# Optimization experiments

Measured on AMD Instinct MI355X. Metric: run time of the kernel, lower is better.

The kernel has to match this reference:

```python
import jax, jax.numpy as jnp
from jax import lax
import numpy as np

B, T, NL = 512, 64, 32          # batch, timepoints per patient, n_labs
LAT, HID = 64, 128              # latent_dim, hidden_dim
SCALE, STEP, QPAD, TMAX = 365.0, 0.05, 2000, 2000


def setup_inputs() -> dict:
    key = jax.random.key(0)
    k = jax.random.split(key, 24)
    def rn(ki, shape, s=0.05):
        return jax.random.normal(ki, shape, jnp.float32) * s
    Din = 2 * NL + 1  # GRU input: labs, mask, dt
    return {
        "obs_vals": rn(k[0], (B, T, NL), 1.0),
        "age": jax.random.uniform(k[1], (B,), jnp.float32),
        "eps": rn(k[2], (B, LAT), 1.0),  # reparameterization noise (randn_like)
        "gru_Wih": rn(k[3], (Din, 3 * HID)), "gru_Whh": rn(k[4], (HID, 3 * HID)),
        "gru_bih": jnp.zeros((3 * HID,)), "gru_bhh": jnp.zeros((3 * HID,)),
        "Wmu": rn(k[5], (HID, LAT)), "bmu": jnp.zeros((LAT,)),
        "Wlv": rn(k[6], (HID, LAT)), "blv": jnp.zeros((LAT,)),
        "W1": rn(k[7], (LAT, HID)), "b1": jnp.zeros((HID,)),
        "W2": rn(k[8], (HID, HID)), "b2": jnp.zeros((HID,)),
        "W3": rn(k[9], (HID, LAT)), "b3": jnp.zeros((LAT,)),
        "Wo1": rn(k[10], (LAT, HID)), "bo1": jnp.zeros((HID,)),
        "Wo2": rn(k[11], (HID, NL)), "bo2": jnp.zeros((NL,)),
        "Ws1": rn(k[12], (LAT + 1, HID)), "bs1": jnp.zeros((HID,)),
        "Ws2": rn(k[13], (HID, 2)), "bs2": jnp.zeros((2,)),
        "obs_mask": jax.random.bernoulli(k[14], 0.7, (B, T, NL)),
        "timepoints": jnp.sort(jax.random.randint(k[15], (B, T), 0, TMAX), axis=1).astype(jnp.int32),
        "seq_lens": jax.random.randint(k[16], (B,), 1, T + 1).astype(jnp.int32),
    }


def reference(obs_vals, age, eps, gru_Wih, gru_Whh, gru_bih, gru_bhh,
              Wmu, bmu, Wlv, blv, W1, b1, W2, b2, W3, b3,
              Wo1, bo1, Wo2, bo2, Ws1, bs1, Ws2, bs2,
              obs_mask, timepoints, seq_lens):
    Bv, Tv, Dv = obs_vals.shape
    Hdim = gru_Whh.shape[0]
    tp = timepoints.astype(jnp.float32)

    # ---- RecognitionRNN (GRU over reversed sequence) ----
    dt = jnp.concatenate([jnp.zeros((Bv, 1)), tp[:, 1:] - tp[:, :-1]], axis=1)[..., None]
    maskf = obs_mask.astype(obs_vals.dtype)
    inp = jnp.concatenate([obs_vals * maskf, maskf, dt], axis=-1)  # [B,T,2*NL+1]
    x_seq = jnp.flip(inp, axis=1).transpose(1, 0, 2)  # [T,B,Din]

    def gru_step(h, x):
        gi = x @ gru_Wih + gru_bih
        gh = h @ gru_Whh + gru_bhh
        ir, iz, i_n = jnp.split(gi, 3, axis=-1)
        hr, hz, hn = jnp.split(gh, 3, axis=-1)
        r = jax.nn.sigmoid(ir + hr)
        zg = jax.nn.sigmoid(iz + hz)
        n = jnp.tanh(i_n + r * hn)
        h = (1.0 - zg) * n + zg * h
        return h, None

    h, _ = lax.scan(gru_step, jnp.zeros((Bv, Hdim), obs_vals.dtype), x_seq)
    mu = h @ Wmu + bmu
    logvar = h @ Wlv + blv
    z0 = mu + eps * jnp.exp(0.5 * logvar)  # reparameterize

    # ---- query times (padded unique; timepoints are >= 0 by construction) ----
    qd = jnp.unique(timepoints.reshape(-1), size=QPAD, fill_value=timepoints.max())
    query_t = qd.astype(jnp.float32) / SCALE  # [Q], nondecreasing

    # ---- torchdiffeq fixed-grid rk4 with step_size ----
    qnp = np.asarray(query_t)
    t0, t1 = float(qnp[0]), float(qnp[-1])
    niters = int(np.ceil((t1 - t0) / STEP + 1))
    grid = np.arange(niters) * STEP + t0
    if grid[-1] > t1:
        grid[-1] = t1
    grid = jnp.asarray(grid, jnp.float32)  # [G]

    def ode_f(z):
        return jnp.tanh(jnp.tanh(z @ W1 + b1) @ W2 + b2) @ W3 + b3

    def rk4_step(y, hstep):
        k1 = ode_f(y)
        k2 = ode_f(y + 0.5 * hstep * k1)
        k3 = ode_f(y + 0.5 * hstep * k2)
        k4 = ode_f(y + hstep * k3)
        y2 = y + (hstep / 6.0) * (k1 + 2.0 * k2 + 2.0 * k3 + k4)
        return y2, y2

    _, ys = lax.scan(rk4_step, z0, grid[1:] - grid[:-1])
    ys = jnp.concatenate([z0[None], ys], axis=0)  # [G,B,L]

    # linear interpolation of grid states at query_t (torchdiffeq behavior)
    gi = jnp.clip(jnp.searchsorted(grid, query_t, side="right") - 1, 0, grid.shape[0] - 2)
    tl, tr = grid[gi], grid[gi + 1]
    w = ((query_t - tl) / jnp.where(tr - tl == 0, 1.0, tr - tl))[:, None, None]
    z_traj = ys[gi] * (1.0 - w) + ys[gi + 1] * w  # [Q,B,L]

    # ---- reconstruction loss (vectorized over B,T) ----
    tq = tp / SCALE  # [B,T]
    idx_q = jnp.argmin(jnp.abs(query_t[None, None, :] - tq[:, :, None]), axis=-1)  # [B,T]
    z_bt = z_traj[idx_q, jnp.arange(Bv)[:, None]]  # [B,T,L]
    x_hat = jax.nn.relu(z_bt @ Wo1 + bo1) @ Wo2 + bo2  # [B,T,NL]
    valid = (jnp.arange(Tv)[None, :] < seq_lens[:, None]).astype(obs_vals.dtype)[..., None]
    m = maskf * valid
    n_obs = m.sum()
    recon = jnp.where(n_obs > 0,
                      (m * (x_hat - obs_vals) ** 2).sum() / jnp.maximum(n_obs, 1.0),
                      0.0)

    kl = -0.5 * jnp.mean(jnp.sum(1.0 + logvar - mu ** 2 - jnp.exp(logvar), axis=-1))

    # ---- z_eval at last observed timepoint per patient ----
    last_tp = jnp.take_along_axis(tp, (seq_lens - 1)[:, None], axis=1)[:, 0] / SCALE  # [B]
    idx_e = jnp.argmin(jnp.abs(query_t[None, :] - last_tp[:, None]), axis=-1)  # [B]
    z_eval = z_traj[idx_e, jnp.arange(Bv)]  # [B,L]
    log_hazard = jax.nn.relu(jnp.concatenate([z_eval, age[:, None]], axis=-1) @ Ws1 + bs1) @ Ws2 + bs2
    return log_hazard, recon, kl, z_eval
```

## Files before the change

### kernel.cpp

```cpp
#include <hip/hip_runtime.h>
#include <hip/hip_bf16.h>
#include <math.h>

#define B 512
#define T 64
#define NL 32
#define LAT 64
#define HID 128
#define DIN 65
#define G3 384
#define FSCALE 365.0f
#define MAXGRID 128

#define WS_MIN   0
#define WS_MAX   1
#define WS_NIT   2
#define WS_KL    3
#define WS_RE    4
#define WS_NO    5
#define WS_GRID  8
#define WS_Z0    (WS_GRID + MAXGRID)
#define WS_YS    (WS_Z0 + B*LAT)
#define WS_W31   (WS_YS + 120*B*LAT)
#define WS_B31   (WS_W31 + HID*HID)

typedef __attribute__((ext_vector_type(8))) __bf16 bf16x8;
typedef __attribute__((ext_vector_type(4))) float f32x4;

#define SWZ(row) ((((row)>>3)&1)<<5)

static __device__ __forceinline__ float tanh_fast(float x){
    float t = __builtin_amdgcn_exp2f(x * 2.8853900817779268f);
    return 1.0f - 2.0f * __builtin_amdgcn_rcpf(t + 1.0f);
}
static __device__ __forceinline__ float sigmoid_fast(float x){
    return __builtin_amdgcn_rcpf(1.0f + __builtin_amdgcn_exp2f(-1.4426950408889634f * x));
}
static __device__ __forceinline__ void bar_lds(){
    asm volatile("" ::: "memory");
    asm volatile("s_waitcnt lgkmcnt(0)" ::: "memory");
    __builtin_amdgcn_s_barrier();
    asm volatile("" ::: "memory");
}

__global__ void k_setup(const int* __restrict__ tp, float* wsf){
    int* wsi = (int*)wsf;
    __shared__ int smin[256], smax[256];
    int tid = threadIdx.x;
    int mn = 2147483647, mx = -2147483647-1;
    for (int i = tid; i < B*T; i += 256){ int v = tp[i]; mn = min(mn,v); mx = max(mx,v); }
    smin[tid]=mn; smax[tid]=mx; __syncthreads();
    for (int s=128; s>0; s>>=1){
        if (tid<s){ smin[tid]=min(smin[tid],smin[tid+s]); smax[tid]=max(smax[tid],smax[tid+s]); }
        __syncthreads();
    }
    float t0f = (float)smin[0] / FSCALE;
    float t1f = (float)smax[0] / FSCALE;
    double t0d = (double)t0f, t1d = (double)t1f;
    int nit = (int)ceil((t1d-t0d)/0.05 + 1.0);
    if (nit < 1) nit = 1;
    if (nit > MAXGRID) nit = MAXGRID;
    if (tid==0){
        wsi[WS_NIT] = nit;
        wsf[WS_KL]=0.f; wsf[WS_RE]=0.f; wsf[WS_NO]=0.f;
    }
    if (tid < nit){
        double g = (double)tid * 0.05 + t0d;
        if (tid == nit-1 && g > t1d) g = t1d;
        wsf[WS_GRID + tid] = (float)g;
    }
}

__global__ __launch_bounds__(256) void k_w31(
    const float* __restrict__ W1, const float* __restrict__ W3,
    const float* __restrict__ b3, float* wsf)
{
    int gid = blockIdx.x*256 + threadIdx.x;
    int k = gid >> 5, n0 = (gid & 31)*4;
    float4 acc = {0.f,0.f,0.f,0.f};
    #pragma unroll 8
    for (int l=0;l<64;++l){
        float w3v = W3[k*LAT + l];
        float4 w1v = *(const float4*)&W1[l*HID + n0];
        acc.x = fmaf(w3v, w1v.x, acc.x);
        acc.y = fmaf(w3v, w1v.y, acc.y);
        acc.z = fmaf(w3v, w1v.z, acc.z);
        acc.w = fmaf(w3v, w1v.w, acc.w);
    }
    *(float4*)&wsf[WS_W31 + k*HID + n0] = acc;
    if (blockIdx.x==0 && threadIdx.x < HID){
        int n = threadIdx.x; float a = 0.f;
        #pragma unroll 8
        for (int l=0;l<64;++l) a = fmaf(b3[l], W1[l*HID+n], a);
        wsf[WS_B31 + n] = a;
    }
}

__global__ __launch_bounds__(512) void k_gru(
    const float* __restrict__ obs, const float* __restrict__ eps,
    const float* __restrict__ Wih, const float* __restrict__ Whh,
    const float* __restrict__ bih, const float* __restrict__ bhh,
    const float* __restrict__ Wmu, const float* __restrict__ bmu,
    const float* __restrict__ Wlv, const float* __restrict__ blv,
    const int* __restrict__ maskI, const int* __restrict__ tp,
    float* wsf)
{
    const int b0 = blockIdx.x * 16;
    const int tid = threadIdx.x;
    const int w = tid >> 6, lane = tid & 63;
    const int g = lane >> 4, c = lane & 15;
    const int xr = tid >> 5, xl = tid & 31;

    __shared__ __align__(16) __bf16 xh[16][232];
    __shared__ int   tps[16][64];
    __shared__ float dts[16];
    __shared__ float lvs[16][64];
    __shared__ float red[8];
    char* xbase = (char*)&xh[0][0];
    #define XH_RD(row, bytecol) (*(const bf16x8*)(xbase + (row)*464 + ((bytecol) ^ SWZ(row))))
    #define XH_WPTR(row, bytecol) ((__bf16*)(xbase + (row)*464 + ((bytecol) ^ SWZ(row))))

    ((int2*)tps)[tid] = ((const int2*)(tp + (size_t)b0*T))[tid];
    {
        unsigned* xz = (unsigned*)xbase;
        #pragma unroll
        for (int i=0;i<1856;i+=512) xz[i+tid] = 0u;
    }

    bf16x8 wr[6], wz[6], wi[2], wh[4];
    #pragma unroll
    for (int q=0;q<6;++q){
        int kt = q<2 ? q : q+1;
        #pragma unroll
        for (int e=0;e<8;++e){
            int k = kt*32 + g*8 + e;
            float vr, vz;
            if (k < 64){ vr = Wih[k*G3 + 16*w+c];      vz = Wih[k*G3 + 128+16*w+c]; }
            else       { vr = Whh[(k-96)*G3 + 16*w+c]; vz = Whh[(k-96)*G3 + 128+16*w+c]; }
            wr[q][e] = (__bf16)vr; wz[q][e] = (__bf16)vz;
        }
    }
    #pragma unroll
    for (int q=0;q<2;++q)
        #pragma unroll
        for (int e=0;e<8;++e)
            wi[q][e] = (__bf16)Wih[(q*32+g*8+e)*G3 + 256+16*w+c];
    #pragma unroll
    for (int q=0;q<4;++q)
        #pragma unroll
        for (int e=0;e<8;++e)
            wh[q][e] = (__bf16)Whh[(q*32+g*8+e)*G3 + 256+16*w+c];
    const float wdr = Wih[64*G3 + 16*w+c];
    const float wdz = Wih[64*G3 + 128+16*w+c];
    const float wdn = Wih[64*G3 + 256+16*w+c];
    const float rb  = bih[16*w+c]     + bhh[16*w+c];
    const float zb  = bih[128+16*w+c] + bhh[128+16*w+c];
    const float inb = bih[256+16*w+c];
    const float hnb = bhh[256+16*w+c];

    __syncthreads();

    {
        float mv = (float)maskI[((size_t)(b0+xr)*T + 63)*NL + xl];
        float ov = obs[((size_t)(b0+xr)*T + 63)*NL + xl];
        *XH_WPTR(xr, 2*xl)      = (__bf16)(ov*mv);
        *XH_WPTR(xr, 64 + 2*xl) = (__bf16)mv;
        if (xl==0) dts[xr] = (float)(tps[xr][63]-tps[xr][62]);
    }
    float ovP = 0.f, mvP = 0.f;
    {
        mvP = (float)maskI[((size_t)(b0+xr)*T + 62)*NL + xl];
        ovP = obs[((size_t)(b0+xr)*T + 62)*NL + xl];
    }

    float hold[4] = {0.f,0.f,0.f,0.f};

    for (int s=0;s<T;++s){
        bar_lds();
        bf16x8 A0 = XH_RD(c, 0   + 16*g);
        bf16x8 A1 = XH_RD(c, 64  + 16*g);
        bf16x8 A2 = XH_RD(c, 192 + 16*g);
        bf16x8 A3 = XH_RD(c, 256 + 16*g);
        bf16x8 A4 = XH_RD(c, 320 + 16*g);
        bf16x8 A5 = XH_RD(c, 384 + 16*g);
        const float dt0=dts[4*g], dt1=dts[4*g+1], dt2=dts[4*g+2], dt3=dts[4*g+3];
        float ovN=0.f, mvN=0.f; const int t2 = 61-s;
        if (t2 >= 0){
            mvN = (float)maskI[((size_t)(b0+xr)*T + t2)*NL + xl];
            ovN = obs[((size_t)(b0+xr)*T + t2)*NL + xl];
        }
        f32x4 racc={0,0,0,0}, zacc={0,0,0,0}, inacc={0,0,0,0}, hnacc={0,0,0,0};
        racc  = __builtin_amdgcn_mfma_f32_16x16x32_bf16(A0, wr[0], racc, 0,0,0);
        zacc  = __builtin_amdgcn_mfma_f32_16x16x32_bf16(A0, wz[0], zacc, 0,0,0);
        inacc = __builtin_amdgcn_mfma_f32_16x16x32_bf16(A0, wi[0], inacc,0,0,0);
        hnacc = __builtin_amdgcn_mfma_f32_16x16x32_bf16(A2, wh[0], hnacc,0,0,0);
        racc  = __builtin_amdgcn_mfma_f32_16x16x32_bf16(A1, wr[1], racc, 0,0,0);
        zacc  = __builtin_amdgcn_mfma_f32_16x16x32_bf16(A1, wz[1], zacc, 0,0,0);
        inacc = __builtin_amdgcn_mfma_f32_16x16x32_bf16(A1, wi[1], inacc,0,0,0);
        hnacc = __builtin_amdgcn_mfma_f32_16x16x32_bf16(A3, wh[1], hnacc,0,0,0);
        racc  = __builtin_amdgcn_mfma_f32_16x16x32_bf16(A2, wr[2], racc, 0,0,0);
        zacc  = __builtin_amdgcn_mfma_f32_16x16x32_bf16(A2, wz[2], zacc, 0,0,0);
        hnacc = __builtin_amdgcn_mfma_f32_16x16x32_bf16(A4, wh[2], hnacc,0,0,0);
        racc  = __builtin_amdgcn_mfma_f32_16x16x32_bf16(A3, wr[3], racc, 0,0,0);
        zacc  = __builtin_amdgcn_mfma_f32_16x16x32_bf16(A3, wz[3], zacc, 0,0,0);
        hnacc = __builtin_amdgcn_mfma_f32_16x16x32_bf16(A5, wh[3], hnacc,0,0,0);
        racc  = __builtin_amdgcn_mfma_f32_16x16x32_bf16(A4, wr[4], racc, 0,0,0);
        zacc  = __builtin_amdgcn_mfma_f32_16x16x32_bf16(A4, wz[4], zacc, 0,0,0);
        racc  = __builtin_amdgcn_mfma_f32_16x16x32_bf16(A5, wr[5], racc, 0,0,0);
        zacc  = __builtin_amdgcn_mfma_f32_16x16x32_bf16(A5, wz[5], zacc, 0,0,0);
        float hnew[4]; const float dtv[4] = {dt0,dt1,dt2,dt3};
        #pragma unroll
        for (int j=0;j<4;++j){
            float dv = dtv[j];
            float r  = sigmoid_fast(racc[j] + rb + dv*wdr);
            float zg = sigmoid_fast(zacc[j] + zb + dv*wdz);
            float n  = tanh_fast(inacc[j] + inb + dv*wdn + r*(hnacc[j] + hnb));
            float hv = (1.f - zg)*n + zg*hold[j];
            hold[j] = hv; hnew[j] = hv;
        }
        bar_lds();
        #pragma unroll
        for (int j=0;j<4;++j)
            *XH_WPTR(4*g+j, 192 + 2*(16*w+c)) = (__bf16)hnew[j];
        if (s < T-1){
            const int tn = 62 - s;
            *XH_WPTR(xr, 2*xl)      = (__bf16)(ovP*mvP);
            *XH_WPTR(xr, 64 + 2*xl) = (__bf16)mvP;
            if (xl==0) dts[xr] = (tn>0) ? (float)(tps[xr][tn]-tps[xr][tn-1]) : 0.f;
        }
        ovP = ovN; mvP = mvN;
    }
    __syncthreads();

    const int col4 = 16*(w&3)+c;
    bf16x8 Ah0 = XH_RD(c, 192 + 0   + 16*g);
    bf16x8 Ah1 = XH_RD(c, 192 + 64  + 16*g);
    bf16x8 Ah2 = XH_RD(c, 192 + 128 + 16*g);
    bf16x8 Ah3 = XH_RD(c, 192 + 192 + 16*g);
    const float* Wm = (w<4)? Wmu : Wlv;
    f32x4 acc={0,0,0,0};
    {
        bf16x8 bf0,bf1,bf2,bf3;
        #pragma unroll
        for (int e=0;e<8;++e){
            bf0[e] = (__bf16)Wm[(0*32+g*8+e)*LAT + col4];
            bf1[e] = (__bf16)Wm[(1*32+g*8+e)*LAT + col4];
            bf2[e] = (__bf16)Wm[(2*32+g*8+e)*LAT + col4];
            bf3[e] = (__bf16)Wm[(3*32+g*8+e)*LAT + col4];
        }
        acc = __builtin_amdgcn_mfma_f32_16x16x32_bf16(Ah0, bf0, acc, 0,0,0);
        acc = __builtin_amdgcn_mfma_f32_16x16x32_bf16(Ah1, bf1, acc, 0,0,0);
        acc = __builtin_amdgcn_mfma_f32_16x16x32_bf16(Ah2, bf2, acc, 0,0,0);
        acc = __builtin_amdgcn_mfma_f32_16x16x32_bf16(Ah3, bf3, acc, 0,0,0);
    }
    const float mbias = (w<4)? bmu[col4] : blv[col4];
    if (w>=4){
        #pragma unroll
        for (int j=0;j<4;++j) lvs[4*g+j][col4] = acc[j] + mbias;
    }
    __syncthreads();
    if (w<4){
        float kl = 0.f;
        #pragma unroll
        for (int j=0;j<4;++j){
            float mu = acc[j] + mbias;
            float lv = lvs[4*g+j][col4];
            int row = b0 + 4*g + j;
            float z0 = mu + eps[(size_t)row*LAT + col4]*expf(0.5f*lv);
            wsf[WS_Z0 + (size_t)row*LAT + col4] = z0;
            wsf[WS_YS + (size_t)row*LAT + col4] = z0;
            kl += 1.f + lv - mu*mu - expf(lv);
        }
        #pragma unroll
        for (int off=32; off>0; off>>=1) kl += __shfl_xor(kl, off);
        if (lane==0) red[w] = kl;
    }
    __syncthreads();
    if (tid==0) atomicAdd(&wsf[WS_KL], red[0]+red[1]+red[2]+red[3]);
    #undef XH_RD
    #undef XH_WPTR
}

__global__ __launch_bounds__(512) void k_ode(
    const float* __restrict__ W1, const float* __restrict__ b1,
    const float* __restrict__ W2, const float* __restrict__ b2,
    const float* __restrict__ W3, const float* __restrict__ b3,
    float* wsf)
{
    const int b0 = blockIdx.x * 16;
    const int tid = threadIdx.x;
    const int w = tid >> 6, lane = tid & 63;
    const int g = lane >> 4, c = lane & 15;
    const int hc = 16*w + c;
    const int lc = 16*(w&3) + c;
    const int* wsi = (const int*)wsf;
    const int nit = wsi[WS_NIT];

    __shared__ __align__(16) __bf16 Gl[16][136];
    __shared__ __align__(16) __bf16 Hl[16][136];
    __shared__ float gls[MAXGRID];
    char* gbase = (char*)&Gl[0][0];
    char* hbase = (char*)&Hl[0][0];
    #define LDS_RD(base, row, bytecol) (*(const bf16x8*)((base) + (row)*272 + ((bytecol) ^ SWZ(row))))
    #define LDS_WPTR(base, row, bytecol) ((__bf16*)((base) + (row)*272 + ((bytecol) ^ SWZ(row))))

    bf16x8 w2f[4], w31f[4], w3f[4];
    #pragma unroll
    for (int q=0;q<4;++q)
        #pragma unroll
        for (int e=0;e<8;++e){
            w2f[q][e]  = (__bf16)W2[(q*32+g*8+e)*HID + hc];
            w31f[q][e] = (__bf16)wsf[WS_W31 + (q*32+g*8+e)*HID + hc];
            w3f[q][e]  = (__bf16)W3[(q*32+g*8+e)*LAT + lc];
        }
    const float b1v  = b1[hc];
    const float b2v  = b2[hc];
    const float b31v = wsf[WS_B31 + hc];
    const float b3v  = b3[lc];

    for (int kk=tid; kk<MAXGRID; kk+=512) gls[kk]=wsf[WS_GRID+kk];

    {
        int r = tid >> 5, l0 = (tid & 31)*2;
        float2 zv = *(const float2*)&wsf[WS_Z0 + (size_t)(b0+r)*LAT + l0];
        __bf16* p = LDS_WPTR(gbase, r, 2*l0);
        p[0] = (__bf16)zv.x;
        p[1] = (__bf16)zv.y;
    }
    float y[4];
    #pragma unroll
    for (int j=0;j<4;++j)
        y[j] = wsf[WS_Z0 + (size_t)(b0+4*g+j)*LAT + lc];
    __syncthreads();

    f32x4 U;
    {
        bf16x8 az0 = LDS_RD(gbase, c, 16*g);
        bf16x8 az1 = LDS_RD(gbase, c, 64 + 16*g);
        bf16x8 wf0, wf1;
        #pragma unroll
        for (int e=0;e<8;++e){
            wf0[e] = (__bf16)W1[(g*8+e)*HID + hc];
            wf1[e] = (__bf16)W1[(32+g*8+e)*HID + hc];
        }
        f32x4 a = {0.f,0.f,0.f,0.f};
        a = __builtin_amdgcn_mfma_f32_16x16x32_bf16(az0, wf0, a, 0,0,0);
        a = __builtin_amdgcn_mfma_f32_16x16x32_bf16(az1, wf1, a, 0,0,0);
        U = a;
    }
    __syncthreads();

    #pragma unroll
    for (int j=0;j<4;++j)
        *LDS_WPTR(gbase, 4*g+j, 2*hc) = (__bf16)tanh_fast(U[j] + b1v);
    __syncthreads();

    f32x4 Uacc={0,0,0,0}, faccv={0,0,0,0};

    for (int i=0; i<nit-1; ++i){
        const float h = gls[i+1]-gls[i];
        #pragma unroll
        for (int sub=0; sub<4; ++sub){
            {
                bf16x8 a0 = LDS_RD(gbase, c, 0   + 16*g);
                bf16x8 a1 = LDS_RD(gbase, c, 64  + 16*g);
                bf16x8 a2 = LDS_RD(gbase, c, 128 + 16*g);
                bf16x8 a3 = LDS_RD(gbase, c, 192 + 16*g);
                __builtin_amdgcn_s_setprio(1);
                f32x4 ca={0,0,0,0}, cb={0,0,0,0};
                ca = __builtin_amdgcn_mfma_f32_16x16x32_bf16(a0, w2f[0], ca, 0,0,0);
                cb = __builtin_amdgcn_mfma_f32_16x16x32_bf16(a2, w2f[2], cb, 0,0,0);
                ca = __builtin_amdgcn_mfma_f32_16x16x32_bf16(a1, w2f[1], ca, 0,0,0);
                cb = __builtin_amdgcn_mfma_f32_16x16x32_bf16(a3, w2f[3], cb, 0,0,0);
                __builtin_amdgcn_s_setprio(0);
                #pragma unroll
                for (int j=0;j<4;++j)
                    *LDS_WPTR(hbase, 4*g+j, 2*hc) = (__bf16)tanh_fast(ca[j]+cb[j]+b2v);
            }
            bar_lds();
            {
                bf16x8 h0 = LDS_RD(hbase, c, 0   + 16*g);
                bf16x8 h1 = LDS_RD(hbase, c, 64  + 16*g);
                bf16x8 h2 = LDS_RD(hbase, c, 128 + 16*g);
                bf16x8 h3 = LDS_RD(hbase, c, 192 + 16*g);
                __builtin_amdgcn_s_setprio(1);
                f32x4 va={0,0,0,0}, vb={0,0,0,0};
                va = __builtin_amdgcn_mfma_f32_16x16x32_bf16(h0, w31f[0], va, 0,0,0);
                vb = __builtin_amdgcn_mfma_f32_16x16x32_bf16(h2, w31f[2], vb, 0,0,0);
                va = __builtin_amdgcn_mfma_f32_16x16x32_bf16(h1, w31f[1], va, 0,0,0);
                vb = __builtin_amdgcn_mfma_f32_16x16x32_bf16(h3, w31f[3], vb, 0,0,0);
                f32x4 fv = {0,0,0,0};
                if (w < 4){
                    f32x4 fa={0,0,0,0}, fb={0,0,0,0};
                    fa = __builtin_amdgcn_mfma_f32_16x16x32_bf16(h0, w3f[0], fa, 0,0,0);
                    fb = __builtin_amdgcn_mfma_f32_16x16x32_bf16(h2, w3f[2], fb, 0,0,0);
                    fa = __builtin_amdgcn_mfma_f32_16x16x32_bf16(h1, w3f[1], fa, 0,0,0);
                    fb = __builtin_amdgcn_mfma_f32_16x16x32_bf16(h3, w3f[3], fb, 0,0,0);
                    #pragma unroll
                    for (int j=0;j<4;++j) fv[j] = fa[j] + fb[j] + b3v;
                }
                __builtin_amdgcn_s_setprio(0);
                f32x4 V;
                #pragma unroll
                for (int j=0;j<4;++j) V[j] = va[j] + vb[j] + b31v;

                if (sub==0){ Uacc = V; faccv = fv; }
                else if (sub==3){ Uacc += V; faccv += fv; }
                else { Uacc += 2.f*V; faccv += 2.f*fv; }

                if (sub < 3){
                    const float al = (sub==2) ? h : 0.5f*h;
                    #pragma unroll
                    for (int j=0;j<4;++j)
                        *LDS_WPTR(gbase, 4*g+j, 2*hc) = (__bf16)tanh_fast(fmaf(al, V[j], U[j]) + b1v);
                } else {
                    const float h6 = h*(1.0f/6.0f);
                    if (w < 4){
                        #pragma unroll
                        for (int j=0;j<4;++j){
                            y[j] = fmaf(h6, faccv[j], y[j]);
                            wsf[WS_YS + ((size_t)(i+1)*B + (b0+4*g+j))*LAT + lc] = y[j];
                        }
                    }
                    #pragma unroll
                    for (int j=0;j<4;++j){
                        U[j] = fmaf(h6, Uacc[j], U[j]);
                        *LDS_WPTR(gbase, 4*g+j, 2*hc) = (__bf16)tanh_fast(U[j] + b1v);
                    }
                }
            }
            bar_lds();
        }
    }
    #undef LDS_RD
    #undef LDS_WPTR
}

__global__ __launch_bounds__(512) void k_recon(
    const float* __restrict__ obs, const int* __restrict__ maskI,
    const int* __restrict__ tp, const int* __restrict__ seq,
    const float* __restrict__ Wo1, const float* __restrict__ bo1,
    const float* __restrict__ Wo2, const float* __restrict__ bo2,
    const float* __restrict__ age,
    const float* __restrict__ Ws1, const float* __restrict__ bs1,
    const float* __restrict__ Ws2, const float* __restrict__ bs2,
    float* wsf, float* out)
{
    const int b = blockIdx.x, tid = threadIdx.x;
    const int w = tid >> 6, lane = tid & 63;
    const int g = lane >> 4, c = lane & 15;
    __shared__ __align__(16) __bf16 zbt[64][72];
    __shared__ __align__(16) __bf16 hb[64][136];
    __shared__ float gls[MAXGRID];
    __shared__ float red[16];
    __shared__ float ze[64];
    __shared__ float pred[4];
    const int* wsi=(const int*)wsf;
    const int nit = wsi[WS_NIT];
    for (int i=tid;i<MAXGRID;i+=512) gls[i]=wsf[WS_GRID+i];

    bf16x8 wo1f[2], wo2f[4];
    #pragma unroll
    for (int q=0;q<2;++q)
        #pragma unroll
        for (int e=0;e<8;++e)
            wo1f[q][e] = (__bf16)Wo1[(q*32+g*8+e)*HID + 16*w+c];
    {
        int n = w & 1;
        #pragma unroll
        for (int q=0;q<4;++q)
            #pragma unroll
            for (int e=0;e<8;++e)
                wo2f[q][e] = (__bf16)Wo2[(q*32+g*8+e)*NL + 16*n+c];
    }
    const float bo1v = bo1[16*w+c];
    const float bo2v = bo2[16*(w&1)+c];
    const int sl = seq[b];
    __syncthreads();

    {
        int t = tid >> 3, seg = tid & 7;
        float tq = (float)tp[b*T+t] / FSCALE;
        int lo=0, hi=nit;
        while (lo<hi){ int mid=(lo+hi)>>1; if (gls[mid]<=tq) lo=mid+1; else hi=mid; }
        int k = lo-1; if (k<0) k=0; if (nit>=2 && k>nit-2) k=nit-2; if (nit<2) k=0;
        float wq=0.f;
        if (nit>=2){ float tl=gls[k], tr=gls[k+1]; float den=(tr-tl==0.f)?1.f:(tr-tl); wq=(tq-tl)/den; }
        size_t o0 = (size_t)WS_YS + ((size_t)k*B + b)*LAT + seg*8;
        float4 za0 = *(const float4*)&wsf[o0];
        float4 za1 = *(const float4*)&wsf[o0+4];
        float4 zb0, zb1;
        if (nit>=2){
            zb0 = *(const float4*)&wsf[o0 + (size_t)B*LAT];
            zb1 = *(const float4*)&wsf[o0 + (size_t)B*LAT + 4];
        } else { zb0 = za0; zb1 = za1; }
        __bf16* dst = &zbt[t][seg*8];
        dst[0] = (__bf16)(za0.x*(1.f-wq)+zb0.x*wq);
        dst[1] = (__bf16)(za0.y*(1.f-wq)+zb0.y*wq);
        dst[2] = (__bf16)(za0.z*(1.f-wq)+zb0.z*wq);
        dst[3] = (__bf16)(za0.w*(1.f-wq)+zb0.w*wq);
        dst[4] = (__bf16)(za1.x*(1.f-wq)+zb1.x*wq);
        dst[5] = (__bf16)(za1.y*(1.f-wq)+zb1.y*wq);
        dst[6] = (__bf16)(za1.z*(1.f-wq)+zb1.z*wq);
        dst[7] = (__bf16)(za1.w*(1.f-wq)+zb1.w*wq);
    }
    __syncthreads();

    #pragma unroll
    for (int m=0;m<4;++m){
        f32x4 acc = {0.f,0.f,0.f,0.f};
        bf16x8 a0 = *(const bf16x8*)&zbt[16*m+c][g*8];
        bf16x8 a1 = *(const bf16x8*)&zbt[16*m+c][32+g*8];
        acc = __builtin_amdgcn_mfma_f32_16x16x32_bf16(a0, wo1f[0], acc, 0,0,0);
        acc = __builtin_amdgcn_mfma_f32_16x16x32_bf16(a1, wo1f[1], acc, 0,0,0);
        #pragma unroll
        for (int j=0;j<4;++j)
            hb[16*m+4*g+j][16*w+c] = (__bf16)fmaxf(acc[j] + bo1v, 0.f);
    }
    __syncthreads();

    float esum = 0.f, ncnt = 0.f;
    {
        int m = w >> 1, n = w & 1;
        f32x4 ca = {0.f,0.f,0.f,0.f}, cb = {0.f,0.f,0.f,0.f};
        bf16x8 a0 = *(const bf16x8*)&hb[16*m+c][g*8];
        bf16x8 a1 = *(const bf16x8*)&hb[16*m+c][32+g*8];
        bf16x8 a2 = *(const bf16x8*)&hb[16*m+c][64+g*8];
        bf16x8 a3 = *(const bf16x8*)&hb[16*m+c][96+g*8];
        ca = __builtin_amdgcn_mfma_f32_16x16x32_bf16(a0, wo2f[0], ca, 0,0,0);
        cb = __builtin_amdgcn_mfma_f32_16x16x32_bf16(a2, wo2f[2], cb, 0,0,0);
        ca = __builtin_amdgcn_mfma_f32_16x16x32_bf16(a1, wo2f[1], ca, 0,0,0);
        cb = __builtin_amdgcn_mfma_f32_16x16x32_bf16(a3, wo2f[3], cb, 0,0,0);
        #pragma unroll
        for (int j=0;j<4;++j){
            int t = 16*m + 4*g + j;
            int col = 16*n + c;
            float xh2 = (ca[j]+cb[j]) + bo2v;
            float mv = (float)maskI[(b*T+t)*NL+col] * ((t<sl)?1.f:0.f);
            float d = xh2 - obs[(b*T+t)*NL+col];
            esum = fmaf(mv*d, d, esum);
            ncnt += mv;
        }
    }
    #pragma unroll
    for (int off=32; off>0; off>>=1){
        esum += __shfl_xor(esum, off);
        ncnt += __shfl_xor(ncnt, off);
    }
    if (lane==0){ red[w] = esum; red[8+w] = ncnt; }
    __syncthreads();
    if (tid==0){
        float s=0.f, nn=0.f;
        #pragma unroll
        for (int i=0;i<8;++i){ s += red[i]; nn += red[8+i]; }
        atomicAdd(&wsf[WS_RE], s);
        atomicAdd(&wsf[WS_NO], nn);
    }

    {
        float tq = (float)tp[b*T + sl-1] / FSCALE;
        int lo=0,hi=nit;
        while(lo<hi){int mid=(lo+hi)>>1; if (gls[mid]<=tq) lo=mid+1; else hi=mid;}
        int k=lo-1; if(k<0)k=0; if(nit>=2 && k>nit-2)k=nit-2; if (nit<2) k=0;
        float wq=0.f;
        if (nit>=2){ float tl=gls[k],tr=gls[k+1]; float den=(tr-tl==0.f)?1.f:(tr-tl); wq=(tq-tl)/den; }
        if (tid<LAT){
            size_t o0 = (size_t)WS_YS + ((size_t)k*B+b)*LAT+tid;
            float zl = wsf[o0]*(1.f-wq) + ((nit>=2)? wsf[o0+(size_t)B*LAT]*wq : 0.f);
            ze[tid]=zl;
            out[1026 + b*LAT + tid] = zl;
        }
        __syncthreads();
        if (tid < 128){
            float hj = bs1[tid];
            #pragma unroll 8
            for (int l=0;l<LAT;++l) hj = fmaf(ze[l], Ws1[l*HID+tid], hj);
            hj = fmaf(age[b], Ws1[LAT*HID+tid], hj);
            hj = fmaxf(hj,0.f);
            float p0 = hj*Ws2[tid*2+0], p1 = hj*Ws2[tid*2+1];
            #pragma unroll
            for (int off=32;off>0;off>>=1){ p0 += __shfl_down(p0,off); p1 += __shfl_down(p1,off); }
            int wv = tid>>6;
            if ((tid&63)==0){ pred[wv*2]=p0; pred[wv*2+1]=p1; }
        }
        __syncthreads();
        if (tid==0){
            out[b*2+0] = bs2[0] + pred[0]+pred[2];
            out[b*2+1] = bs2[1] + pred[1]+pred[3];
        }
    }
}

__global__ void k_fin(float* wsf, float* out){
    float n = wsf[WS_NO];
    out[1024] = (n>0.f) ? (wsf[WS_RE]/fmaxf(n,1.f)) : 0.f;
    out[1025] = -0.5f * (wsf[WS_KL] / (float)B);
}

extern "C" void kernel_launch(void* const* d_in, const int* in_sizes, int n_in,
                              void* d_out, int out_size, void* d_ws, size_t ws_size,
                              hipStream_t stream) {
    const float* obs   = (const float*)d_in[0];
    const float* age   = (const float*)d_in[1];
    const float* eps   = (const float*)d_in[2];
    const float* Wih   = (const float*)d_in[3];
    const float* Whh   = (const float*)d_in[4];
    const float* bih   = (const float*)d_in[5];
    const float* bhh   = (const float*)d_in[6];
    const float* Wmu   = (const float*)d_in[7];
    const float* bmu   = (const float*)d_in[8];
    const float* Wlv   = (const float*)d_in[9];
    const float* blv   = (const float*)d_in[10];
    const float* W1    = (const float*)d_in[11];
    const float* b1    = (const float*)d_in[12];
    const float* W2    = (const float*)d_in[13];
    const float* b2    = (const float*)d_in[14];
    const float* W3    = (const float*)d_in[15];
    const float* b3    = (const float*)d_in[16];
    const float* Wo1   = (const float*)d_in[17];
    const float* bo1   = (const float*)d_in[18];
    const float* Wo2   = (const float*)d_in[19];
    const float* bo2   = (const float*)d_in[20];
    const float* Ws1   = (const float*)d_in[21];
    const float* bs1   = (const float*)d_in[22];
    const float* Ws2   = (const float*)d_in[23];
    const float* bs2   = (const float*)d_in[24];
    const int*   maskI = (const int*)d_in[25];
    const int*   tp    = (const int*)d_in[26];
    const int*   seq   = (const int*)d_in[27];
    float* wsf = (float*)d_ws;
    float* out = (float*)d_out;

    k_setup<<<1, 256, 0, stream>>>(tp, wsf);
    k_w31<<<16, 256, 0, stream>>>(W1, W3, b3, wsf);
    k_gru<<<B/16, 512, 0, stream>>>(obs, eps, Wih, Whh, bih, bhh, Wmu, bmu, Wlv, blv,
                                    maskI, tp, wsf);
    k_ode<<<B/16, 512, 0, stream>>>(W1, b1, W2, b2, W3, b3, wsf);
    k_recon<<<B, 512, 0, stream>>>(obs, maskI, tp, seq, Wo1, bo1, Wo2, bo2,
                                   age, Ws1, bs1, Ws2, bs2, wsf, out);
    k_fin<<<1, 1, 0, stream>>>(wsf, out);
}
```

Baseline: 527.8 us.

## Prepack bf16 weight fragments in a prep kernel and fold finalize into recon

Merges the setup and W3·W1 product kernels into one prep kernel that also converts the GRU, ODE and recon weights into bf16 MFMA fragment layouts in the workspace. The main kernels then load their fragments with one contiguous 16-byte read per thread instead of many strided scalar global loads and conversions per block. The separate finalize kernel is removed: the last recon block, found through an atomic counter, writes the loss scalars. This cuts two kernel launches and the redundant per-block weight gathering. It adds a workspace dependency, and the combined W31 is now rounded to bf16 in a different order.

```diff
diff --git a/kernel.cpp b/kernel.cpp
--- a/kernel.cpp
+++ b/kernel.cpp
@@ -12,17 +12,19 @@
 #define FSCALE 365.0f
 #define MAXGRID 128
 
-#define WS_MIN   0
-#define WS_MAX   1
 #define WS_NIT   2
 #define WS_KL    3
 #define WS_RE    4
 #define WS_NO    5
+#define WS_CNT   6
 #define WS_GRID  8
 #define WS_Z0    (WS_GRID + MAXGRID)
 #define WS_YS    (WS_Z0 + B*LAT)
-#define WS_W31   (WS_YS + 120*B*LAT)
-#define WS_B31   (WS_W31 + HID*HID)
+#define FR_BASE  (WS_YS + 112*B*LAT)
+#define GRU_FR   FR_BASE
+#define ODE_FR   (GRU_FR + 18*512*4)
+#define REC_FR   (ODE_FR + 14*512*4)
+#define WS_B31   (WS_YS + 120*B*LAT)
 
 typedef __attribute__((ext_vector_type(8))) __bf16 bf16x8;
 typedef __attribute__((ext_vector_type(4))) float f32x4;
@@ -43,63 +45,146 @@
     asm volatile("" ::: "memory");
 }
 
-__global__ void k_setup(const int* __restrict__ tp, float* wsf){
+__global__ __launch_bounds__(256) void k_prep(
+    const int* __restrict__ tp,
+    const float* __restrict__ Wih, const float* __restrict__ Whh,
+    const float* __restrict__ W1,  const float* __restrict__ W2,
+    const float* __restrict__ W3,  const float* __restrict__ b3,
+    const float* __restrict__ Wo1, const float* __restrict__ Wo2,
+    float* wsf)
+{
     int* wsi = (int*)wsf;
-    __shared__ int smin[256], smax[256];
-    int tid = threadIdx.x;
-    int mn = 2147483647, mx = -2147483647-1;
-    for (int i = tid; i < B*T; i += 256){ int v = tp[i]; mn = min(mn,v); mx = max(mx,v); }
-    smin[tid]=mn; smax[tid]=mx; __syncthreads();
-    for (int s=128; s>0; s>>=1){
-        if (tid<s){ smin[tid]=min(smin[tid],smin[tid+s]); smax[tid]=max(smax[tid],smax[tid+s]); }
-        __syncthreads();
-    }
-    float t0f = (float)smin[0] / FSCALE;
-    float t1f = (float)smax[0] / FSCALE;
-    double t0d = (double)t0f, t1d = (double)t1f;
-    int nit = (int)ceil((t1d-t0d)/0.05 + 1.0);
-    if (nit < 1) nit = 1;
-    if (nit > MAXGRID) nit = MAXGRID;
-    if (tid==0){
-        wsi[WS_NIT] = nit;
-        wsf[WS_KL]=0.f; wsf[WS_RE]=0.f; wsf[WS_NO]=0.f;
-    }
-    if (tid < nit){
-        double g = (double)tid * 0.05 + t0d;
-        if (tid == nit-1 && g > t1d) g = t1d;
-        wsf[WS_GRID + tid] = (float)g;
-    }
-}
-
-__global__ __launch_bounds__(256) void k_w31(
-    const float* __restrict__ W1, const float* __restrict__ W3,
-    const float* __restrict__ b3, float* wsf)
-{
-    int gid = blockIdx.x*256 + threadIdx.x;
-    int k = gid >> 5, n0 = (gid & 31)*4;
-    float4 acc = {0.f,0.f,0.f,0.f};
-    #pragma unroll 8
-    for (int l=0;l<64;++l){
-        float w3v = W3[k*LAT + l];
-        float4 w1v = *(const float4*)&W1[l*HID + n0];
-        acc.x = fmaf(w3v, w1v.x, acc.x);
-        acc.y = fmaf(w3v, w1v.y, acc.y);
-        acc.z = fmaf(w3v, w1v.z, acc.z);
-        acc.w = fmaf(w3v, w1v.w, acc.w);
-    }
-    *(float4*)&wsf[WS_W31 + k*HID + n0] = acc;
-    if (blockIdx.x==0 && threadIdx.x < HID){
-        int n = threadIdx.x; float a = 0.f;
+    const int tid = threadIdx.x;
+    if (blockIdx.x == 8){
+        __shared__ int smin[256], smax[256];
+        int mn = 2147483647, mx = -2147483647-1;
+        for (int i = tid; i < B*T; i += 256){ int v = tp[i]; mn = min(mn,v); mx = max(mx,v); }
+        smin[tid]=mn; smax[tid]=mx; __syncthreads();
+        for (int s=128; s>0; s>>=1){
+            if (tid<s){ smin[tid]=min(smin[tid],smin[tid+s]); smax[tid]=max(smax[tid],smax[tid+s]); }
+            __syncthreads();
+        }
+        float t0f = (float)smin[0] / FSCALE;
+        float t1f = (float)smax[0] / FSCALE;
+        double t0d = (double)t0f, t1d = (double)t1f;
+        int nit = (int)ceil((t1d-t0d)/0.05 + 1.0);
+        if (nit < 1) nit = 1;
+        if (nit > MAXGRID) nit = MAXGRID;
+        if (tid==0){
+            wsi[WS_NIT] = nit; wsi[WS_CNT] = 0;
+            wsf[WS_KL]=0.f; wsf[WS_RE]=0.f; wsf[WS_NO]=0.f;
+        }
+        if (tid < nit){
+            double g = (double)tid * 0.05 + t0d;
+            if (tid == nit-1 && g > t1d) g = t1d;
+            wsf[WS_GRID + tid] = (float)g;
+        }
+        return;
+    }
+    const int w = blockIdx.x;
+    const int qp = tid >> 6;
+    const int lane = tid & 63;
+    const int g = lane >> 4, c = lane & 15;
+    const int hc = 16*w + c;
+    const int lc = 16*(w&3) + c;
+    const int role = w*64 + lane;
+    __shared__ float W1l[64][HID];
+    __shared__ float W3l[HID][64];
+    for (int i = tid; i < 64*HID/4; i += 256)
+        ((float4*)&W1l[0][0])[i] = ((const float4*)W1)[i];
+    for (int i = tid; i < HID*64/4; i += 256)
+        ((float4*)&W3l[0][0])[i] = ((const float4*)W3)[i];
+    __syncthreads();
+
+    {
+        int qlist[2]; int nq = 0;
+        qlist[nq++] = qp;
+        if (qp < 2) qlist[nq++] = 4+qp;
+        for (int ii=0; ii<nq; ++ii){
+            int q = qlist[ii];
+            int kt = q<2 ? q : q+1;
+            bf16x8 vr8, vz8;
+            #pragma unroll
+            for (int e=0;e<8;++e){
+                int k = kt*32 + g*8 + e;
+                float vr, vz;
+                if (k < 64){ vr = Wih[k*G3 + hc];      vz = Wih[k*G3 + 128+hc]; }
+                else       { vr = Whh[(k-96)*G3 + hc]; vz = Whh[(k-96)*G3 + 128+hc]; }
+                vr8[e] = (__bf16)vr; vz8[e] = (__bf16)vz;
+            }
+            *(bf16x8*)&wsf[GRU_FR + ((q)*512 + role)*4]   = vr8;
+            *(bf16x8*)&wsf[GRU_FR + ((6+q)*512 + role)*4] = vz8;
+        }
+    }
+    if (qp < 2){
+        bf16x8 v;
+        #pragma unroll
+        for (int e=0;e<8;++e) v[e] = (__bf16)Wih[(qp*32+g*8+e)*G3 + 256+hc];
+        *(bf16x8*)&wsf[GRU_FR + ((12+qp)*512 + role)*4] = v;
+    }
+    {
+        bf16x8 v;
+        #pragma unroll
+        for (int e=0;e<8;++e) v[e] = (__bf16)Whh[(qp*32+g*8+e)*G3 + 256+hc];
+        *(bf16x8*)&wsf[GRU_FR + ((14+qp)*512 + role)*4] = v;
+    }
+    {
+        bf16x8 v;
+        #pragma unroll
+        for (int e=0;e<8;++e) v[e] = (__bf16)W2[(qp*32+g*8+e)*HID + hc];
+        *(bf16x8*)&wsf[ODE_FR + ((qp)*512 + role)*4] = v;
+    }
+    {
+        bf16x8 v;
+        #pragma unroll
+        for (int e=0;e<8;++e){
+            int k = qp*32 + g*8 + e;
+            float a0=0.f, a1=0.f;
+            #pragma unroll 4
+            for (int l=0;l<64;l+=2){
+                a0 = fmaf(W3l[k][l],   W1l[l][hc],   a0);
+                a1 = fmaf(W3l[k][l+1], W1l[l+1][hc], a1);
+            }
+            v[e] = (__bf16)(a0+a1);
+        }
+        *(bf16x8*)&wsf[ODE_FR + ((4+qp)*512 + role)*4] = v;
+    }
+    {
+        bf16x8 v;
+        #pragma unroll
+        for (int e=0;e<8;++e) v[e] = (__bf16)W3l[qp*32+g*8+e][lc];
+        *(bf16x8*)&wsf[ODE_FR + ((8+qp)*512 + role)*4] = v;
+    }
+    if (qp < 2){
+        bf16x8 v;
+        #pragma unroll
+        for (int e=0;e<8;++e) v[e] = (__bf16)W1l[qp*32+g*8+e][hc];
+        *(bf16x8*)&wsf[ODE_FR + ((12+qp)*512 + role)*4] = v;
+    }
+    if (qp < 2){
+        bf16x8 v;
+        #pragma unroll
+        for (int e=0;e<8;++e) v[e] = (__bf16)Wo1[(qp*32+g*8+e)*HID + hc];
+        *(bf16x8*)&wsf[REC_FR + ((qp)*512 + role)*4] = v;
+    }
+    {
+        bf16x8 v;
+        #pragma unroll
+        for (int e=0;e<8;++e) v[e] = (__bf16)Wo2[(qp*32+g*8+e)*NL + 16*(w&1)+c];
+        *(bf16x8*)&wsf[REC_FR + ((2+qp)*512 + role)*4] = v;
+    }
+    if (qp == 3 && g == 0){
+        float a = 0.f;
         #pragma unroll 8
-        for (int l=0;l<64;++l) a = fmaf(b3[l], W1[l*HID+n], a);
-        wsf[WS_B31 + n] = a;
+        for (int l=0;l<64;++l) a = fmaf(b3[l], W1l[l][hc], a);
+        wsf[WS_B31 + hc] = a;
     }
 }
 
 __global__ __launch_bounds__(512) void k_gru(
     const float* __restrict__ obs, const float* __restrict__ eps,
-    const float* __restrict__ Wih, const float* __restrict__ Whh,
     const float* __restrict__ bih, const float* __restrict__ bhh,
+    const float* __restrict__ Wih,
     const float* __restrict__ Wmu, const float* __restrict__ bmu,
     const float* __restrict__ Wlv, const float* __restrict__ blv,
     const int* __restrict__ maskI, const int* __restrict__ tp,
@@ -128,28 +213,17 @@
     }
 
     bf16x8 wr[6], wz[6], wi[2], wh[4];
-    #pragma unroll
-    for (int q=0;q<6;++q){
-        int kt = q<2 ? q : q+1;
-        #pragma unroll
-        for (int e=0;e<8;++e){
-            int k = kt*32 + g*8 + e;
-            float vr, vz;
-            if (k < 64){ vr = Wih[k*G3 + 16*w+c];      vz = Wih[k*G3 + 128+16*w+c]; }
-            else       { vr = Whh[(k-96)*G3 + 16*w+c]; vz = Whh[(k-96)*G3 + 128+16*w+c]; }
-            wr[q][e] = (__bf16)vr; wz[q][e] = (__bf16)vz;
-        }
-    }
-    #pragma unroll
-    for (int q=0;q<2;++q)
-        #pragma unroll
-        for (int e=0;e<8;++e)
-            wi[q][e] = (__bf16)Wih[(q*32+g*8+e)*G3 + 256+16*w+c];
-    #pragma unroll
-    for (int q=0;q<4;++q)
-        #pragma unroll
-        for (int e=0;e<8;++e)
-            wh[q][e] = (__bf16)Whh[(q*32+g*8+e)*G3 + 256+16*w+c];
+    {
+        const bf16x8* gfr = (const bf16x8*)&wsf[GRU_FR];
+        #pragma unroll
+        for (int q=0;q<6;++q) wr[q] = gfr[q*512 + tid];
+        #pragma unroll
+        for (int q=0;q<6;++q) wz[q] = gfr[(6+q)*512 + tid];
+        #pragma unroll
+        for (int q=0;q<2;++q) wi[q] = gfr[(12+q)*512 + tid];
+        #pragma unroll
+        for (int q=0;q<4;++q) wh[q] = gfr[(14+q)*512 + tid];
+    }
     const float wdr = Wih[64*G3 + 16*w+c];
     const float wdz = Wih[64*G3 + 128+16*w+c];
     const float wdn = Wih[64*G3 + 256+16*w+c];
@@ -282,10 +356,8 @@
 }
 
 __global__ __launch_bounds__(512) void k_ode(
-    const float* __restrict__ W1, const float* __restrict__ b1,
-    const float* __restrict__ W2, const float* __restrict__ b2,
-    const float* __restrict__ W3, const float* __restrict__ b3,
-    float* wsf)
+    const float* __restrict__ b1, const float* __restrict__ b2,
+    const float* __restrict__ b3, float* wsf)
 {
     const int b0 = blockIdx.x * 16;
     const int tid = threadIdx.x;
@@ -304,15 +376,18 @@
     #define LDS_RD(base, row, bytecol) (*(const bf16x8*)((base) + (row)*272 + ((bytecol) ^ SWZ(row))))
     #define LDS_WPTR(base, row, bytecol) ((__bf16*)((base) + (row)*272 + ((bytecol) ^ SWZ(row))))
 
-    bf16x8 w2f[4], w31f[4], w3f[4];
-    #pragma unroll
-    for (int q=0;q<4;++q)
-        #pragma unroll
-        for (int e=0;e<8;++e){
-            w2f[q][e]  = (__bf16)W2[(q*32+g*8+e)*HID + hc];
-            w31f[q][e] = (__bf16)wsf[WS_W31 + (q*32+g*8+e)*HID + hc];
-            w3f[q][e]  = (__bf16)W3[(q*32+g*8+e)*LAT + lc];
-        }
+    bf16x8 w2f[4], w31f[4], w3f[4], w1f0, w1f1;
+    {
+        const bf16x8* ofr = (const bf16x8*)&wsf[ODE_FR];
+        #pragma unroll
+        for (int q=0;q<4;++q) w2f[q]  = ofr[q*512 + tid];
+        #pragma unroll
+        for (int q=0;q<4;++q) w31f[q] = ofr[(4+q)*512 + tid];
+        #pragma unroll
+        for (int q=0;q<4;++q) w3f[q]  = ofr[(8+q)*512 + tid];
+        w1f0 = ofr[12*512 + tid];
+        w1f1 = ofr[13*512 + tid];
+    }
     const float b1v  = b1[hc];
     const float b2v  = b2[hc];
     const float b31v = wsf[WS_B31 + hc];
@@ -337,15 +412,9 @@
     {
         bf16x8 az0 = LDS_RD(gbase, c, 16*g);
         bf16x8 az1 = LDS_RD(gbase, c, 64 + 16*g);
-        bf16x8 wf0, wf1;
-        #pragma unroll
-        for (int e=0;e<8;++e){
-            wf0[e] = (__bf16)W1[(g*8+e)*HID + hc];
-            wf1[e] = (__bf16)W1[(32+g*8+e)*HID + hc];
-        }
         f32x4 a = {0.f,0.f,0.f,0.f};
-        a = __builtin_amdgcn_mfma_f32_16x16x32_bf16(az0, wf0, a, 0,0,0);
-        a = __builtin_amdgcn_mfma_f32_16x16x32_bf16(az1, wf1, a, 0,0,0);
+        a = __builtin_amdgcn_mfma_f32_16x16x32_bf16(az0, w1f0, a, 0,0,0);
+        a = __builtin_amdgcn_mfma_f32_16x16x32_bf16(az1, w1f1, a, 0,0,0);
         U = a;
     }
     __syncthreads();
@@ -439,8 +508,7 @@
 __global__ __launch_bounds__(512) void k_recon(
     const float* __restrict__ obs, const int* __restrict__ maskI,
     const int* __restrict__ tp, const int* __restrict__ seq,
-    const float* __restrict__ Wo1, const float* __restrict__ bo1,
-    const float* __restrict__ Wo2, const float* __restrict__ bo2,
+    const float* __restrict__ bo1, const float* __restrict__ bo2,
     const float* __restrict__ age,
     const float* __restrict__ Ws1, const float* __restrict__ bs1,
     const float* __restrict__ Ws2, const float* __restrict__ bs2,
@@ -460,18 +528,12 @@
     for (int i=tid;i<MAXGRID;i+=512) gls[i]=wsf[WS_GRID+i];
 
     bf16x8 wo1f[2], wo2f[4];
-    #pragma unroll
-    for (int q=0;q<2;++q)
-        #pragma unroll
-        for (int e=0;e<8;++e)
-            wo1f[q][e] = (__bf16)Wo1[(q*32+g*8+e)*HID + 16*w+c];
-    {
-        int n = w & 1;
-        #pragma unroll
-        for (int q=0;q<4;++q)
-            #pragma unroll
-            for (int e=0;e<8;++e)
-                wo2f[q][e] = (__bf16)Wo2[(q*32+g*8+e)*NL + 16*n+c];
+    {
+        const bf16x8* rfr = (const bf16x8*)&wsf[REC_FR];
+        wo1f[0] = rfr[0*512 + tid];
+        wo1f[1] = rfr[1*512 + tid];
+        #pragma unroll
+        for (int q=0;q<4;++q) wo2f[q] = rfr[(2+q)*512 + tid];
     }
     const float bo1v = bo1[16*w+c];
     const float bo2v = bo2[16*(w&1)+c];
@@ -589,12 +651,18 @@
             out[b*2+1] = bs2[1] + pred[1]+pred[3];
         }
     }
-}
-
-__global__ void k_fin(float* wsf, float* out){
-    float n = wsf[WS_NO];
-    out[1024] = (n>0.f) ? (wsf[WS_RE]/fmaxf(n,1.f)) : 0.f;
-    out[1025] = -0.5f * (wsf[WS_KL] / (float)B);
+
+    if (tid==0){
+        __threadfence();
+        int prev = atomicAdd((int*)wsf + WS_CNT, 1);
+        if (prev == B-1){
+            float re = atomicAdd(&wsf[WS_RE], 0.f);
+            float no = atomicAdd(&wsf[WS_NO], 0.f);
+            float kl = atomicAdd(&wsf[WS_KL], 0.f);
+            out[1024] = (no>0.f) ? (re/fmaxf(no,1.f)) : 0.f;
+            out[1025] = -0.5f * (kl / (float)B);
+        }
+    }
 }
 
 extern "C" void kernel_launch(void* const* d_in, const int* in_sizes, int n_in,
@@ -631,12 +699,10 @@
     float* wsf = (float*)d_ws;
     float* out = (float*)d_out;
 
-    k_setup<<<1, 256, 0, stream>>>(tp, wsf);
-    k_w31<<<16, 256, 0, stream>>>(W1, W3, b3, wsf);
-    k_gru<<<B/16, 512, 0, stream>>>(obs, eps, Wih, Whh, bih, bhh, Wmu, bmu, Wlv, blv,
+    k_prep<<<9, 256, 0, stream>>>(tp, Wih, Whh, W1, W2, W3, b3, Wo1, Wo2, wsf);
+    k_gru<<<B/16, 512, 0, stream>>>(obs, eps, bih, bhh, Wih, Wmu, bmu, Wlv, blv,
                                     maskI, tp, wsf);
-    k_ode<<<B/16, 512, 0, stream>>>(W1, b1, W2, b2, W3, b3, wsf);
-    k_recon<<<B, 512, 0, stream>>>(obs, maskI, tp, seq, Wo1, bo1, Wo2, bo2,
+    k_ode<<<B/16, 512, 0, stream>>>(b1, b2, b3, wsf);
+    k_recon<<<B, 512, 0, stream>>>(obs, maskI, tp, seq, bo1, bo2,
                                    age, Ws1, bs1, Ws2, bs2, wsf, out);
-    k_fin<<<1, 1, 0, stream>>>(wsf, out);
 }
```

Result: no change. 523.8 us (-0.7%).
